# Kernel optimization log

Measured on AMD Instinct MI355X. Metric: run time of the kernel, lower is better.

The kernel has to match this reference:

```python
import jax, jax.numpy as jnp
import numpy as np

TEMPERATURE = 0.5
EPS = 1e-8  # torch.nn.CosineSimilarity default eps


def setup_inputs() -> dict:
    key = jax.random.key(0)
    k1, k2 = jax.random.split(key)
    B, D = 4096, 256
    z1 = jax.random.normal(k1, (B, D), dtype=jnp.float32)
    # z2 = perturbed view of z1 so positive cosine sims are positive
    # (original torch code takes log of the RAW cosine sim, which is NaN
    #  for negative positives; realistic SimCLR positives are correlated views)
    z2 = z1 + 0.1 * jax.random.normal(k2, (B, D), dtype=jnp.float32)
    return {"z1": z1, "z2": z2}


def reference(z1, z2):
    B = z1.shape[0]
    z = jnp.concatenate([z1, z2], axis=0)                      # [2B, D]
    norm = jnp.maximum(jnp.linalg.norm(z, axis=-1, keepdims=True), EPS)
    zn = z / norm
    sim = zn @ zn.T                                            # [2B, 2B] cosine sims
    # positives: sim[i, i+B] and sim[i+B, i] (RAW cosine, per original code)
    pos = jnp.concatenate([jnp.diagonal(sim, offset=B),
                           jnp.diagonal(sim, offset=-B)])      # [2B]
    # mask self-similarity diagonal to -inf before exp-sum
    diag = jnp.eye(2 * B, dtype=bool)
    sim_masked = jnp.where(diag, -jnp.inf, sim)
    denom = jnp.sum(jnp.exp(sim_masked / TEMPERATURE), axis=-1)  # [2B]
    loss = -jnp.mean(jnp.log(pos / denom))
    return loss
```

## Files before the change

kernel.cpp:

```cpp
#include <hip/hip_runtime.h>
#include <hip/hip_bf16.h>


#define NROWS 8192
#define BHALF 4096
#define DDIM  256

typedef __attribute__((ext_vector_type(4))) int   i32x4;
typedef __attribute__((ext_vector_type(8))) int   i32x8;
typedef __attribute__((ext_vector_type(4))) float f32x4;

#define SCALE1 0x7F7F7F7F
#define TWO_LOG2E 2.8853900817779268f

__device__ __forceinline__ void load_lds16(const unsigned char* g, unsigned char* l) {
    __builtin_amdgcn_global_load_lds(
        (const __attribute__((address_space(1))) void*)g,
        (__attribute__((address_space(3))) void*)l, 16, 0, 0);
}

__global__ __launch_bounds__(256) void prep_kernel(const float* __restrict__ z1,
                                                   const float* __restrict__ z2,
                                                   unsigned char* __restrict__ zn8,
                                                   float* __restrict__ posPart,
                                                   float* __restrict__ denom,
                                                   float* __restrict__ out) {
    __shared__ float sp[4];
    int wave = threadIdx.x >> 6;
    int lane = threadIdx.x & 63;
    int i    = blockIdx.x * 4 + wave;
    float4 a = reinterpret_cast<const float4*>(z1 + (size_t)i * DDIM)[lane];
    float4 b = reinterpret_cast<const float4*>(z2 + (size_t)i * DDIM)[lane];
    float ss1 = a.x * a.x + a.y * a.y + a.z * a.z + a.w * a.w;
    float ss2 = b.x * b.x + b.y * b.y + b.z * b.z + b.w * b.w;
    float dd  = a.x * b.x + a.y * b.y + a.z * b.z + a.w * b.w;
    #pragma unroll
    for (int off = 32; off; off >>= 1) {
        ss1 += __shfl_xor(ss1, off);
        ss2 += __shfl_xor(ss2, off);
        dd  += __shfl_xor(dd, off);
    }
    float n1 = fmaxf(sqrtf(ss1), 1e-8f);
    float n2 = fmaxf(sqrtf(ss2), 1e-8f);
    float i1 = 1.0f / n1, i2 = 1.0f / n2;
    int pa = __builtin_amdgcn_cvt_pk_fp8_f32(a.x * i1, a.y * i1, 0, 0);
    pa     = __builtin_amdgcn_cvt_pk_fp8_f32(a.z * i1, a.w * i1, pa, 1);
    int pb = __builtin_amdgcn_cvt_pk_fp8_f32(b.x * i2, b.y * i2, 0, 0);
    pb     = __builtin_amdgcn_cvt_pk_fp8_f32(b.z * i2, b.w * i2, pb, 1);
    reinterpret_cast<int*>(zn8 + (size_t)i * DDIM)[lane] = pa;
    reinterpret_cast<int*>(zn8 + (size_t)(i + BHALF) * DDIM)[lane] = pb;
    if (lane == 0) sp[wave] = __logf(dd * i1 * i2);
    if (threadIdx.x < 8) denom[blockIdx.x * 8 + threadIdx.x] = 0.0f;
    if (blockIdx.x == 0 && threadIdx.x == 64) out[0] = 0.0f;
    __syncthreads();
    if (threadIdx.x == 0)
        posPart[blockIdx.x] = sp[0] + sp[1] + sp[2] + sp[3];
}

__global__ __launch_bounds__(256, 3) void denom_kernel(const unsigned char* __restrict__ zn8,
                                                       float* __restrict__ denom) {
    __shared__ __align__(16) unsigned char sA[128 * DDIM];
    __shared__ __align__(16) unsigned char sB[64 * DDIM];

    int x = blockIdx.x, y = blockIdx.y;
    int bi, bj;
    if (x > y) { bi = y;      bj = x - 1;  }
    else       { bi = 63 - y; bj = 63 - x; }
    int iBase = bi * 128;
    int jBase = bj * 128;
    bool isDiag = (bi == bj);

    int t    = threadIdx.x;
    int lane = t & 63;
    int wave = t >> 6;
    int col  = lane & 15;
    int quad = lane >> 4;
    int wm = wave >> 1, wn = wave & 1;

    int rowL  = t >> 4;
    int chunk = (t & 15) ^ rowL;
    const unsigned char* gA = zn8 + (size_t)(iBase + rowL) * DDIM + chunk * 16;
    unsigned char* lA = sA + t * 16;
    unsigned char* lB = sB + t * 16;

    #pragma unroll
    for (int s = 0; s < 8; s++)
        load_lds16(gA + s * 4096, lA + s * 4096);
    {
        const unsigned char* gB = zn8 + (size_t)(jBase + rowL) * DDIM + chunk * 16;
        #pragma unroll
        for (int s = 0; s < 4; s++)
            load_lds16(gB + s * 4096, lB + s * 4096);
    }
    __syncthreads();

    float rs[4][4];
    #pragma unroll
    for (int mt = 0; mt < 4; mt++)
        #pragma unroll
        for (int r = 0; r < 4; r++) rs[mt][r] = 0.f;

    const unsigned char* aRow = sA + (size_t)(wm * 64 + col) * DDIM;
    const unsigned char* bRow = sB + (size_t)(wn * 32 + col) * DDIM;

    #pragma unroll
    for (int h = 0; h < 2; h++) {
        if (h) {
            __syncthreads();
            const unsigned char* gB = zn8 + (size_t)(jBase + 64 + rowL) * DDIM + chunk * 16;
            #pragma unroll
            for (int s = 0; s < 4; s++)
                load_lds16(gB + s * 4096, lB + s * 4096);
            __syncthreads();
        }

        i32x8 bfr[2][2];
        #pragma unroll
        for (int nt = 0; nt < 2; nt++) {
            #pragma unroll
            for (int ks = 0; ks < 2; ks++) {
                int g0 = ks * 8 + quad * 2;
                i32x4 lo = *(const i32x4*)(bRow + nt * 16 * DDIM + ((g0    ) ^ col) * 16);
                i32x4 hi = *(const i32x4*)(bRow + nt * 16 * DDIM + ((g0 + 1) ^ col) * 16);
                bfr[nt][ks] = __builtin_shufflevector(lo, hi, 0, 1, 2, 3, 4, 5, 6, 7);
            }
        }

        float cs[2] = {0.f, 0.f};
        #pragma unroll
        for (int mt = 0; mt < 4; mt++) {
            i32x8 af[2];
            #pragma unroll
            for (int ks = 0; ks < 2; ks++) {
                int g0 = ks * 8 + quad * 2;
                i32x4 lo = *(const i32x4*)(aRow + mt * 16 * DDIM + ((g0    ) ^ col) * 16);
                i32x4 hi = *(const i32x4*)(aRow + mt * 16 * DDIM + ((g0 + 1) ^ col) * 16);
                af[ks] = __builtin_shufflevector(lo, hi, 0, 1, 2, 3, 4, 5, 6, 7);
            }
            int gi = iBase + wm * 64 + mt * 16;
            #pragma unroll
            for (int nt = 0; nt < 2; nt++) {
                f32x4 acc = {0.f, 0.f, 0.f, 0.f};
                acc = __builtin_amdgcn_mfma_scale_f32_16x16x128_f8f6f4(
                          af[0], bfr[nt][0], acc, 0, 0, 0, SCALE1, 0, SCALE1);
                acc = __builtin_amdgcn_mfma_scale_f32_16x16x128_f8f6f4(
                          af[1], bfr[nt][1], acc, 0, 0, 0, SCALE1, 0, SCALE1);
                bool dtile = (gi == jBase + h * 64 + wn * 32 + nt * 16);
                float csl = 0.f;
                #pragma unroll
                for (int r = 0; r < 4; r++) {
                    float e = exp2f(acc[r] * TWO_LOG2E);
                    if (dtile && (quad * 4 + r) == col) e = 0.f;
                    rs[mt][r] += e;
                    csl += e;
                }
                cs[nt] += csl;
            }
        }

        if (!isDiag) {
            #pragma unroll
            for (int nt = 0; nt < 2; nt++) {
                float v = cs[nt];
                v += __shfl_xor(v, 16);
                v += __shfl_xor(v, 32);
                if (quad == 0)
                    atomicAdd(&denom[jBase + h * 64 + wn * 32 + nt * 16 + col], v);
            }
        }
    }

    #pragma unroll
    for (int mt = 0; mt < 4; mt++)
        #pragma unroll
        for (int r = 0; r < 4; r++) {
            float v = rs[mt][r];
            v += __shfl_xor(v, 1);
            v += __shfl_xor(v, 2);
            v += __shfl_xor(v, 4);
            v += __shfl_xor(v, 8);
            rs[mt][r] = v;
        }
    __syncthreads();
    float* red = (float*)sA;
    if (col == 0) {
        #pragma unroll
        for (int mt = 0; mt < 4; mt++)
            #pragma unroll
            for (int r = 0; r < 4; r++)
                red[wn * 128 + wm * 64 + mt * 16 + quad * 4 + r] = rs[mt][r];
    }
    __syncthreads();
    if (t < 128)
        atomicAdd(&denom[iBase + t], red[t] + red[128 + t]);
}

__global__ __launch_bounds__(256) void loss_kernel(const float* __restrict__ posPart,
                                                   const float* __restrict__ denom,
                                                   float* __restrict__ out) {
    __shared__ float sdata[4];
    int t = threadIdx.x;
    float s = __logf(denom[blockIdx.x * 256 + t]);
    if (t < 32) s -= 2.0f * posPart[blockIdx.x * 32 + t];
    #pragma unroll
    for (int off = 32; off; off >>= 1) s += __shfl_xor(s, off);
    if ((t & 63) == 0) sdata[t >> 6] = s;
    __syncthreads();
    if (t == 0)
        atomicAdd(out, (sdata[0] + sdata[1] + sdata[2] + sdata[3]) * (1.0f / NROWS));
}

extern "C" void kernel_launch(void* const* d_in, const int* in_sizes, int n_in,
                              void* d_out, int out_size, void* d_ws, size_t ws_size,
                              hipStream_t stream) {
    const float* z1 = (const float*)d_in[0];
    const float* z2 = (const float*)d_in[1];

    unsigned char* zn8 = (unsigned char*)d_ws;
    float* denom   = (float*)((char*)d_ws + (size_t)NROWS * DDIM);
    float* posPart = denom + NROWS;

    prep_kernel<<<BHALF / 4, 256, 0, stream>>>(z1, z2, zn8, posPart, denom, (float*)d_out);
    denom_kernel<<<dim3(65, 32), 256, 0, stream>>>(zn8, denom);
    loss_kernel<<<NROWS / 256, 256, 0, stream>>>(posPart, denom, (float*)d_out);
}
```

Measured before the change: 87.17 us.

## Process multiple column tiles per block with double-buffered B and register-resident A

Each block now keeps its 128-row A tile resident and walks up to four 128-column B tiles along the upper triangle. B half-tiles are double-buffered in LDS so the next load overlaps the current MFMA/exp work. A fragments are loaded into registers once instead of per half-tile. This cuts redundant A loads and launch count, at the cost of higher register/LDS use (occupancy hint lowered to 2), uneven work per row of blocks, and many early-exiting blocks in the launch grid.

```diff
diff --git a/kernel.cpp b/kernel.cpp
--- a/kernel.cpp
+++ b/kernel.cpp
@@ -5,6 +5,7 @@
 #define NROWS 8192
 #define BHALF 4096
 #define DDIM  256
+#define CHUNK 4
 
 typedef __attribute__((ext_vector_type(4))) int   i32x4;
 typedef __attribute__((ext_vector_type(8))) int   i32x8;
@@ -57,18 +58,17 @@
         posPart[blockIdx.x] = sp[0] + sp[1] + sp[2] + sp[3];
 }
 
-__global__ __launch_bounds__(256, 3) void denom_kernel(const unsigned char* __restrict__ zn8,
+__global__ __launch_bounds__(256, 2) void denom_kernel(const unsigned char* __restrict__ zn8,
                                                        float* __restrict__ denom) {
     __shared__ __align__(16) unsigned char sA[128 * DDIM];
-    __shared__ __align__(16) unsigned char sB[64 * DDIM];
-
-    int x = blockIdx.x, y = blockIdx.y;
-    int bi, bj;
-    if (x > y) { bi = y;      bj = x - 1;  }
-    else       { bi = 63 - y; bj = 63 - x; }
+    __shared__ __align__(16) unsigned char sB[2][64 * DDIM];
+
+    int bi  = blockIdx.y;
+    int bj0 = bi + blockIdx.x * CHUNK;
+    if (bj0 > 63) return;
+    int bjEnd = min(bj0 + CHUNK, 64);
+    int S = 2 * (bjEnd - bj0);
     int iBase = bi * 128;
-    int jBase = bj * 128;
-    bool isDiag = (bi == bj);
 
     int t    = threadIdx.x;
     int lane = t & 63;
@@ -79,21 +79,21 @@
 
     int rowL  = t >> 4;
     int chunk = (t & 15) ^ rowL;
-    const unsigned char* gA = zn8 + (size_t)(iBase + rowL) * DDIM + chunk * 16;
-    unsigned char* lA = sA + t * 16;
-    unsigned char* lB = sB + t * 16;
-
-    #pragma unroll
-    for (int s = 0; s < 8; s++)
-        load_lds16(gA + s * 4096, lA + s * 4096);
+
     {
-        const unsigned char* gB = zn8 + (size_t)(jBase + rowL) * DDIM + chunk * 16;
-        #pragma unroll
-        for (int s = 0; s < 4; s++)
-            load_lds16(gB + s * 4096, lB + s * 4096);
-    }
-    __syncthreads();
-
+        const unsigned char* gA = zn8 + (size_t)(iBase + rowL) * DDIM + chunk * 16;
+        unsigned char* lA = sA + t * 16;
+        #pragma unroll
+        for (int q = 0; q < 8; q++)
+            load_lds16(gA + q * 4096, lA + q * 4096);
+        const unsigned char* gB = zn8 + (size_t)(bj0 * 128 + rowL) * DDIM + chunk * 16;
+        unsigned char* lB = sB[0] + t * 16;
+        #pragma unroll
+        for (int q = 0; q < 4; q++)
+            load_lds16(gB + q * 4096, lB + q * 4096);
+    }
+
+    i32x8 af[4][2];
     float rs[4][4];
     #pragma unroll
     for (int mt = 0; mt < 4; mt++)
@@ -101,22 +101,40 @@
         for (int r = 0; r < 4; r++) rs[mt][r] = 0.f;
 
     const unsigned char* aRow = sA + (size_t)(wm * 64 + col) * DDIM;
-    const unsigned char* bRow = sB + (size_t)(wn * 32 + col) * DDIM;
-
-    #pragma unroll
-    for (int h = 0; h < 2; h++) {
-        if (h) {
-            __syncthreads();
-            const unsigned char* gB = zn8 + (size_t)(jBase + 64 + rowL) * DDIM + chunk * 16;
-            #pragma unroll
-            for (int s = 0; s < 4; s++)
-                load_lds16(gB + s * 4096, lB + s * 4096);
-            __syncthreads();
-        }
+
+    for (int s = 0; s < S; s++) {
+        __syncthreads();
+
+        if (s + 1 < S) {
+            int bj = bj0 + ((s + 1) >> 1), h = (s + 1) & 1;
+            const unsigned char* gB =
+                zn8 + (size_t)(bj * 128 + h * 64 + rowL) * DDIM + chunk * 16;
+            unsigned char* lB = sB[(s + 1) & 1] + t * 16;
+            #pragma unroll
+            for (int q = 0; q < 4; q++)
+                load_lds16(gB + q * 4096, lB + q * 4096);
+        }
+
+        if (s == 0) {
+            #pragma unroll
+            for (int mt = 0; mt < 4; mt++)
+                #pragma unroll
+                for (int ks = 0; ks < 2; ks++) {
+                    int g0 = ks * 8 + quad * 2;
+                    i32x4 lo = *(const i32x4*)(aRow + mt * 16 * DDIM + ((g0    ) ^ col) * 16);
+                    i32x4 hi = *(const i32x4*)(aRow + mt * 16 * DDIM + ((g0 + 1) ^ col) * 16);
+                    af[mt][ks] = __builtin_shufflevector(lo, hi, 0, 1, 2, 3, 4, 5, 6, 7);
+                }
+        }
+
+        int bj = bj0 + (s >> 1), h = s & 1;
+        int jBase = bj * 128;
+        bool isDiag = (bj == bi);
+        const unsigned char* bRow = sB[s & 1] + (size_t)(wn * 32 + col) * DDIM;
 
         i32x8 bfr[2][2];
         #pragma unroll
-        for (int nt = 0; nt < 2; nt++) {
+        for (int nt = 0; nt < 2; nt++)
             #pragma unroll
             for (int ks = 0; ks < 2; ks++) {
                 int g0 = ks * 8 + quad * 2;
@@ -124,27 +142,18 @@
                 i32x4 hi = *(const i32x4*)(bRow + nt * 16 * DDIM + ((g0 + 1) ^ col) * 16);
                 bfr[nt][ks] = __builtin_shufflevector(lo, hi, 0, 1, 2, 3, 4, 5, 6, 7);
             }
-        }
 
         float cs[2] = {0.f, 0.f};
         #pragma unroll
         for (int mt = 0; mt < 4; mt++) {
-            i32x8 af[2];
-            #pragma unroll
-            for (int ks = 0; ks < 2; ks++) {
-                int g0 = ks * 8 + quad * 2;
-                i32x4 lo = *(const i32x4*)(aRow + mt * 16 * DDIM + ((g0    ) ^ col) * 16);
-                i32x4 hi = *(const i32x4*)(aRow + mt * 16 * DDIM + ((g0 + 1) ^ col) * 16);
-                af[ks] = __builtin_shufflevector(lo, hi, 0, 1, 2, 3, 4, 5, 6, 7);
-            }
             int gi = iBase + wm * 64 + mt * 16;
             #pragma unroll
             for (int nt = 0; nt < 2; nt++) {
                 f32x4 acc = {0.f, 0.f, 0.f, 0.f};
                 acc = __builtin_amdgcn_mfma_scale_f32_16x16x128_f8f6f4(
-                          af[0], bfr[nt][0], acc, 0, 0, 0, SCALE1, 0, SCALE1);
+                          af[mt][0], bfr[nt][0], acc, 0, 0, 0, SCALE1, 0, SCALE1);
                 acc = __builtin_amdgcn_mfma_scale_f32_16x16x128_f8f6f4(
-                          af[1], bfr[nt][1], acc, 0, 0, 0, SCALE1, 0, SCALE1);
+                          af[mt][1], bfr[nt][1], acc, 0, 0, 0, SCALE1, 0, SCALE1);
                 bool dtile = (gi == jBase + h * 64 + wn * 32 + nt * 16);
                 float csl = 0.f;
                 #pragma unroll
@@ -221,6 +230,6 @@
     float* posPart = denom + NROWS;
 
     prep_kernel<<<BHALF / 4, 256, 0, stream>>>(z1, z2, zn8, posPart, denom, (float*)d_out);
-    denom_kernel<<<dim3(65, 32), 256, 0, stream>>>(zn8, denom);
+    denom_kernel<<<dim3(16, 64), 256, 0, stream>>>(zn8, denom);
     loss_kernel<<<NROWS / 256, 256, 0, stream>>>(posPart, denom, (float*)d_out);
 }
```

New measurement: 98.15 us. 12.6% more time.

## Hoist A fragments to registers and prefetch second B half into freed LDS

Applied to the files above, without the earlier changes.

Loads all A-tile MFMA fragments into registers once, then reuses the A region of LDS as the buffer for the second B half. That second B load is issued before the first half's compute so it overlaps with it, which removes one barrier and the serialized load stall. The cost is more VGPRs for the held A fragments (64 ints per lane), which may hurt occupancy at the 3-blocks-per-CU launch bound. LDS stays at 48KB per block.

```diff
diff --git a/kernel.cpp b/kernel.cpp
--- a/kernel.cpp
+++ b/kernel.cpp
@@ -59,8 +59,10 @@
 
 __global__ __launch_bounds__(256, 3) void denom_kernel(const unsigned char* __restrict__ zn8,
                                                        float* __restrict__ denom) {
-    __shared__ __align__(16) unsigned char sA[128 * DDIM];
-    __shared__ __align__(16) unsigned char sB[64 * DDIM];
+    __shared__ __align__(16) unsigned char sMem[48 * 1024];
+    unsigned char* sA  = sMem;
+    unsigned char* sB0 = sMem + 32768;
+    unsigned char* sB1 = sMem;
 
     int x = blockIdx.x, y = blockIdx.y;
     int bi, bj;
@@ -79,20 +81,40 @@
 
     int rowL  = t >> 4;
     int chunk = (t & 15) ^ rowL;
-    const unsigned char* gA = zn8 + (size_t)(iBase + rowL) * DDIM + chunk * 16;
-    unsigned char* lA = sA + t * 16;
-    unsigned char* lB = sB + t * 16;
-
-    #pragma unroll
-    for (int s = 0; s < 8; s++)
-        load_lds16(gA + s * 4096, lA + s * 4096);
+
     {
+        const unsigned char* gA = zn8 + (size_t)(iBase + rowL) * DDIM + chunk * 16;
+        #pragma unroll
+        for (int q = 0; q < 8; q++)
+            load_lds16(gA + q * 4096, sA + t * 16 + q * 4096);
         const unsigned char* gB = zn8 + (size_t)(jBase + rowL) * DDIM + chunk * 16;
         #pragma unroll
-        for (int s = 0; s < 4; s++)
-            load_lds16(gB + s * 4096, lB + s * 4096);
-    }
-    __syncthreads();
+        for (int q = 0; q < 4; q++)
+            load_lds16(gB + q * 4096, sB0 + t * 16 + q * 4096);
+    }
+    __syncthreads();
+
+    i32x8 af[4][2];
+    {
+        const unsigned char* aRow = sA + (size_t)(wm * 64 + col) * DDIM;
+        #pragma unroll
+        for (int mt = 0; mt < 4; mt++)
+            #pragma unroll
+            for (int ks = 0; ks < 2; ks++) {
+                int g0 = ks * 8 + quad * 2;
+                i32x4 lo = *(const i32x4*)(aRow + mt * 16 * DDIM + ((g0    ) ^ col) * 16);
+                i32x4 hi = *(const i32x4*)(aRow + mt * 16 * DDIM + ((g0 + 1) ^ col) * 16);
+                af[mt][ks] = __builtin_shufflevector(lo, hi, 0, 1, 2, 3, 4, 5, 6, 7);
+            }
+    }
+    __syncthreads();
+
+    {
+        const unsigned char* gB = zn8 + (size_t)(jBase + 64 + rowL) * DDIM + chunk * 16;
+        #pragma unroll
+        for (int q = 0; q < 4; q++)
+            load_lds16(gB + q * 4096, sB1 + t * 16 + q * 4096);
+    }
 
     float rs[4][4];
     #pragma unroll
@@ -100,23 +122,15 @@
         #pragma unroll
         for (int r = 0; r < 4; r++) rs[mt][r] = 0.f;
 
-    const unsigned char* aRow = sA + (size_t)(wm * 64 + col) * DDIM;
-    const unsigned char* bRow = sB + (size_t)(wn * 32 + col) * DDIM;
-
     #pragma unroll
     for (int h = 0; h < 2; h++) {
-        if (h) {
-            __syncthreads();
-            const unsigned char* gB = zn8 + (size_t)(jBase + 64 + rowL) * DDIM + chunk * 16;
-            #pragma unroll
-            for (int s = 0; s < 4; s++)
-                load_lds16(gB + s * 4096, lB + s * 4096);
-            __syncthreads();
-        }
+        if (h) __syncthreads();
+        const unsigned char* bRow =
+            (h ? sB1 : sB0) + (size_t)(wn * 32 + col) * DDIM;
 
         i32x8 bfr[2][2];
         #pragma unroll
-        for (int nt = 0; nt < 2; nt++) {
+        for (int nt = 0; nt < 2; nt++)
             #pragma unroll
             for (int ks = 0; ks < 2; ks++) {
                 int g0 = ks * 8 + quad * 2;
@@ -124,27 +138,18 @@
                 i32x4 hi = *(const i32x4*)(bRow + nt * 16 * DDIM + ((g0 + 1) ^ col) * 16);
                 bfr[nt][ks] = __builtin_shufflevector(lo, hi, 0, 1, 2, 3, 4, 5, 6, 7);
             }
-        }
 
         float cs[2] = {0.f, 0.f};
         #pragma unroll
         for (int mt = 0; mt < 4; mt++) {
-            i32x8 af[2];
-            #pragma unroll
-            for (int ks = 0; ks < 2; ks++) {
-                int g0 = ks * 8 + quad * 2;
-                i32x4 lo = *(const i32x4*)(aRow + mt * 16 * DDIM + ((g0    ) ^ col) * 16);
-                i32x4 hi = *(const i32x4*)(aRow + mt * 16 * DDIM + ((g0 + 1) ^ col) * 16);
-                af[ks] = __builtin_shufflevector(lo, hi, 0, 1, 2, 3, 4, 5, 6, 7);
-            }
             int gi = iBase + wm * 64 + mt * 16;
             #pragma unroll
             for (int nt = 0; nt < 2; nt++) {
                 f32x4 acc = {0.f, 0.f, 0.f, 0.f};
                 acc = __builtin_amdgcn_mfma_scale_f32_16x16x128_f8f6f4(
-                          af[0], bfr[nt][0], acc, 0, 0, 0, SCALE1, 0, SCALE1);
+                          af[mt][0], bfr[nt][0], acc, 0, 0, 0, SCALE1, 0, SCALE1);
                 acc = __builtin_amdgcn_mfma_scale_f32_16x16x128_f8f6f4(
-                          af[1], bfr[nt][1], acc, 0, 0, 0, SCALE1, 0, SCALE1);
+                          af[mt][1], bfr[nt][1], acc, 0, 0, 0, SCALE1, 0, SCALE1);
                 bool dtile = (gi == jBase + h * 64 + wn * 32 + nt * 16);
                 float csl = 0.f;
                 #pragma unroll
@@ -182,7 +187,7 @@
             rs[mt][r] = v;
         }
     __syncthreads();
-    float* red = (float*)sA;
+    float* red = (float*)(sMem + 16384);
     if (col == 0) {
         #pragma unroll
         for (int mt = 0; mt < 4; mt++)
```

Result: no change. 86.31 us (-1.0%).
